# Performance work log

Measured on AMD Instinct MI355X. Metric: run time of the kernel, lower is better.

Reference implementation:

```python
import jax, jax.numpy as jnp
import numpy as np

B, S, IN, IN2, H = 512, 256, 300, 300, 512
FN = 3  # filter_num


def setup_inputs() -> dict:
    key = jax.random.key(0)
    ks = jax.random.split(key, 16)
    def n(k, shape, scale=0.05):
        return jax.random.normal(k, shape, dtype=jnp.float32) * scale
    return {
        "x": jax.random.normal(ks[0], (B, S, IN), dtype=jnp.float32),
        "W_in": n(ks[1], (IN, IN2)), "b_in": n(ks[2], (IN2,)),
        "Wih": n(ks[3], (IN2, 4 * H)), "Whh": n(ks[4], (H, 4 * H)),
        "bih": n(ks[5], (4 * H,)), "bhh": n(ks[6], (4 * H,)),
        "Q": n(ks[7], (H, IN2)), "R": n(ks[8], (IN2, H)),
        "Wc3": n(ks[9], (FN, 1, 3, H)), "bc3": n(ks[10], (FN,)),
        "Wc4": n(ks[11], (FN, 1, 4, H)), "bc4": n(ks[12], (FN,)),
        "Wc5": n(ks[13], (FN, 1, 5, H)), "bc5": n(ks[14], (FN,)),
        "W_lin": n(ks[15], (3 * FN, 2)), "b_lin": jnp.zeros((2,), jnp.float32),
    }


def reference(x, W_in, b_in, Wih, Whh, bih, bhh, Q, R,
              Wc3, bc3, Wc4, bc4, Wc5, bc5, W_lin, b_lin):
    # input projection: [B,S,IN] -> [B,S,IN2]
    xin = jnp.tanh(x @ W_in + b_in)
    xs = jnp.swapaxes(xin, 0, 1)  # [S,B,IN2] for scan
    bsz = x.shape[0]
    h0 = jnp.zeros((bsz, H), x.dtype)
    c0 = jnp.zeros((bsz, H), x.dtype)

    def step(carry, xt):
        ht, Ct = carry
        # mogrify, mog_iterations=2: i=1 odd updates x, i=2 even updates h
        xt = 2.0 * jax.nn.sigmoid(ht @ Q) * xt
        ht = 2.0 * jax.nn.sigmoid(xt @ R) * ht
        gates = xt @ Wih + bih + ht @ Whh + bhh  # [B,4H]
        i, f, g, o = jnp.split(gates, 4, axis=1)
        Ct = jax.nn.sigmoid(f) * Ct + jax.nn.sigmoid(i) * jnp.tanh(g)
        ht = jax.nn.sigmoid(o) * jnp.tanh(Ct)
        return (ht, Ct), ht

    _, hs = jax.lax.scan(step, (h0, c0), xs)  # [S,B,H]
    hmap = jnp.swapaxes(hs, 0, 1)[:, None, :, :]  # [B,1,S,H]

    feats = []
    for w, b in ((Wc3, bc3), (Wc4, bc4), (Wc5, bc5)):
        y = jax.lax.conv_general_dilated(
            hmap, w, (1, 1), 'VALID',
            dimension_numbers=('NCHW', 'OIHW', 'NCHW'))
        y = jax.nn.relu(y + b[None, :, None, None])  # [B,FN,S-fsz+1,1]
        feats.append(jnp.max(y, axis=(2, 3)))  # global max pool -> [B,FN]
    cat = jnp.concatenate(feats, axis=1)  # [B, 3*FN]
    # dropout is identity at inference
    return cat @ W_lin + b_lin  # [B,2]
```

## Files before the change

### kernel.cpp

```cpp
#include <hip/hip_runtime.h>

#define DI __device__ __forceinline__

typedef __attribute__((ext_vector_type(4))) float  f32x4;
typedef __attribute__((ext_vector_type(8))) short  s16x8;
typedef __attribute__((ext_vector_type(8))) __bf16 bf16x8;
typedef unsigned long long u64;

constexpr int S_   = 256;
constexpr int B_   = 512;
constexpr int H_   = 512;
constexpr int KP_  = 320;
constexpr int ALD_ = 832;
constexpr int NRING = 34;
constexpr int NWG  = 256;
constexpr size_t HSLOT = 512 * 512;

constexpr size_t OFF_XIN = 0;
constexpr size_t SZ_XIN  = (size_t)S_ * B_ * KP_ * 2;
constexpr size_t OFF_U   = OFF_XIN + SZ_XIN;
constexpr size_t SZ_U    = (size_t)B_ * S_ * 64 * 4;
constexpr size_t OFF_HS  = OFF_U + SZ_U;
constexpr size_t SZ_HS   = (size_t)NRING * HSLOT * 2;
constexpr size_t OFF_ACT = OFF_HS + SZ_HS;
constexpr size_t SZ_ACT  = (size_t)B_ * ALD_ * 2;
constexpr size_t OFF_HFP = OFF_ACT + SZ_ACT;
constexpr size_t SZ_HFP  = (size_t)B_ * H_ * 4;
constexpr size_t OFF_WPT = OFF_HFP + SZ_HFP;
constexpr size_t SZ_WPT  = (size_t)320 * 320 * 2;
constexpr size_t OFF_QPT = OFF_WPT + SZ_WPT;
constexpr size_t SZ_QPT  = (size_t)320 * 512 * 2;
constexpr size_t OFF_RPT = OFF_QPT + SZ_QPT;
constexpr size_t SZ_RPT  = (size_t)512 * 320 * 2;
constexpr size_t OFF_WGT = OFF_RPT + SZ_RPT;
constexpr size_t SZ_WGT  = (size_t)2048 * 832 * 2;
constexpr size_t OFF_BG  = OFF_WGT + SZ_WGT;
constexpr size_t SZ_BG   = 2048 * 4;
constexpr size_t OFF_VT  = OFF_BG + SZ_BG;
constexpr size_t SZ_VT   = (size_t)64 * 512 * 2;
constexpr size_t OFF_BAR = OFF_VT + SZ_VT;
constexpr size_t SZ_BAR  = 4096;
constexpr size_t WS_NEED = OFF_BAR + SZ_BAR;

DI unsigned short f2bf(float x) {
  unsigned int u = __float_as_uint(x);
  unsigned int r = (u + 0x7FFFu + ((u >> 16) & 1u)) >> 16;
  return (unsigned short)r;
}
DI float bf2f(unsigned short h) { return __uint_as_float(((unsigned int)h) << 16); }

DI float sigm(float x) {
  float e = __builtin_amdgcn_exp2f(x * -1.44269504088896f);
  return __builtin_amdgcn_rcpf(1.0f + e);
}
DI float tanh_(float x) {
  x = fminf(fmaxf(x, -15.0f), 15.0f);
  float e = __builtin_amdgcn_exp2f(x * 2.88539008177793f);
  return (e - 1.0f) * __builtin_amdgcn_rcpf(e + 1.0f);
}
DI bf16x8 asbf(s16x8 v) { return __builtin_bit_cast(bf16x8, v); }

DI u64 ld_sys_u64(const void* p) {
  return __hip_atomic_load((const u64*)p, __ATOMIC_RELAXED, __HIP_MEMORY_SCOPE_SYSTEM);
}
DI void st_sys_u64(void* p, u64 v) {
  __hip_atomic_store((u64*)p, v, __ATOMIC_RELAXED, __HIP_MEMORY_SCOPE_SYSTEM);
}
template<int N> DI void wait_vm() {
  asm volatile("s_waitcnt vmcnt(%0)" :: "n"(N) : "memory");
}

struct a16x8 { u64 lo, hi; };
DI a16x8 ldA(const unsigned short* p) {
  a16x8 r; r.lo = ld_sys_u64(p); r.hi = ld_sys_u64(p + 4); return r;
}
DI void stA_lds(short* dst, a16x8 v) {
  *(u64*)dst = v.lo; *(u64*)(dst + 4) = v.hi;
}

template<int NR>
DI void gemm2(const unsigned short* Ab, int lda,
              const unsigned short* Bb, int ldb,
              short* sA, short* sB, f32x4 acc[2][2])
{
  const int tid  = threadIdx.x;
  const int t2   = tid & 255;
  const int team = tid >> 8;
  const int lane = t2 & 63;
  const int w = t2 >> 6, wm = w >> 1, wn = w & 1;
  const unsigned short* ga = Ab + (t2 >> 2) * lda + (t2 & 3) * 8;
  const unsigned short* gb = Bb + (t2 >> 2) * ldb + (t2 & 3) * 8;
  const int slot  = team * 2048;
  const int arow0 = (wm * 32 + (lane & 15)) * 32 + (lane >> 4) * 8;
  const int brow0 = (wn * 32 + (lane & 15)) * 32 + (lane >> 4) * 8;

  a16x8 a0, a1 = {};
  s16x8 b0, b1 = {};
  a0 = ldA(ga + team * 32);
  b0 = *(const s16x8*)(gb + team * 32);
  if (NR > 1) {
    a1 = ldA(ga + (2 + team) * 32);
    b1 = *(const s16x8*)(gb + (2 + team) * 32);
  }
  stA_lds(&sA[slot + t2 * 8], a0);
  *(s16x8*)&sB[slot + t2 * 8] = b0;
  __syncthreads();
  #pragma unroll
  for (int j = 0; j < NR; ++j) {
    const int cur = (j & 1) * 4096;
    if (j + 2 < NR) {
      const int kt = 2 * (j + 2) + team;
      if ((j & 1) == 0) { a0 = ldA(ga + kt * 32); b0 = *(const s16x8*)(gb + kt * 32); }
      else              { a1 = ldA(ga + kt * 32); b1 = *(const s16x8*)(gb + kt * 32); }
    }
    s16x8 A0 = *(const s16x8*)&sA[cur + slot + arow0];
    s16x8 A1 = *(const s16x8*)&sA[cur + slot + arow0 + 512];
    s16x8 B0 = *(const s16x8*)&sB[cur + slot + brow0];
    s16x8 B1 = *(const s16x8*)&sB[cur + slot + brow0 + 512];
    acc[0][0] = __builtin_amdgcn_mfma_f32_16x16x32_bf16(asbf(A0), asbf(B0), acc[0][0], 0, 0, 0);
    acc[0][1] = __builtin_amdgcn_mfma_f32_16x16x32_bf16(asbf(A0), asbf(B1), acc[0][1], 0, 0, 0);
    acc[1][0] = __builtin_amdgcn_mfma_f32_16x16x32_bf16(asbf(A1), asbf(B0), acc[1][0], 0, 0, 0);
    acc[1][1] = __builtin_amdgcn_mfma_f32_16x16x32_bf16(asbf(A1), asbf(B1), acc[1][1], 0, 0, 0);
    if (j + 1 < NR) {
      const int nxt = ((j + 1) & 1) * 4096;
      if ((j & 1) == 0) { stA_lds(&sA[nxt + slot + t2 * 8], a1); *(s16x8*)&sB[nxt + slot + t2 * 8] = b1; }
      else              { stA_lds(&sA[nxt + slot + t2 * 8], a0); *(s16x8*)&sB[nxt + slot + t2 * 8] = b0; }
    }
    __syncthreads();
  }
}

DI void reduce_teams(f32x4 acc[2][2], float* rbuf) {
  const int tid = threadIdx.x, t2 = tid & 255;
  if (tid >= 256) {
    #pragma unroll
    for (int mi = 0; mi < 2; ++mi)
      #pragma unroll
      for (int ni = 0; ni < 2; ++ni)
        #pragma unroll
        for (int r = 0; r < 4; ++r)
          rbuf[((mi * 2 + ni) * 4 + r) * 256 + t2] = acc[mi][ni][r];
  }
  __syncthreads();
  if (tid < 256) {
    #pragma unroll
    for (int mi = 0; mi < 2; ++mi)
      #pragma unroll
      for (int ni = 0; ni < 2; ++ni)
        #pragma unroll
        for (int r = 0; r < 4; ++r)
          acc[mi][ni][r] += rbuf[((mi * 2 + ni) * 4 + r) * 256 + t2];
  }
}

template<int NK, int KREAL>
DI void gemm_f32A(const float* Af, int lda,
                  const unsigned short* Bb, int ldb,
                  short* sA, short* sB, f32x4 acc[2][2])
{
  const int tid  = threadIdx.x;
  const int lane = tid & 63;
  const int w = tid >> 6, wm = w >> 1, wn = w & 1;
  const float* ga = Af + (tid >> 2) * lda;
  const int cseg  = (tid & 3) * 8;
  const unsigned short* gb = Bb + (tid >> 2) * ldb + (tid & 3) * 8;
  const int arow0 = (wm * 32 + (lane & 15)) * 32 + (lane >> 4) * 8;
  const int brow0 = (wn * 32 + (lane & 15)) * 32 + (lane >> 4) * 8;

  auto loadA = [&](int k) -> s16x8 {
    s16x8 r;
    const int c0 = k * 32 + cseg;
    if (c0 + 8 <= KREAL) {
      float4 f0 = *(const float4*)(ga + c0);
      float4 f1 = *(const float4*)(ga + c0 + 4);
      r[0] = (short)f2bf(f0.x); r[1] = (short)f2bf(f0.y);
      r[2] = (short)f2bf(f0.z); r[3] = (short)f2bf(f0.w);
      r[4] = (short)f2bf(f1.x); r[5] = (short)f2bf(f1.y);
      r[6] = (short)f2bf(f1.z); r[7] = (short)f2bf(f1.w);
    } else {
      #pragma unroll
      for (int j = 0; j < 8; ++j) {
        float x = (c0 + j < KREAL) ? ga[c0 + j] : 0.0f;
        r[j] = (short)f2bf(x);
      }
    }
    return r;
  };

  s16x8 va = loadA(0);
  s16x8 vb = *(const s16x8*)gb;
  *(s16x8*)&sA[tid * 8] = va;
  *(s16x8*)&sB[tid * 8] = vb;
  __syncthreads();
  for (int k = 0; k < NK; ++k) {
    const int cur = (k & 1) * 2048;
    if (k + 1 < NK) {
      va = loadA(k + 1);
      vb = *(const s16x8*)(gb + (k + 1) * 32);
    }
    s16x8 a0 = *(const s16x8*)&sA[cur + arow0];
    s16x8 a1 = *(const s16x8*)&sA[cur + arow0 + 16 * 32];
    s16x8 b0 = *(const s16x8*)&sB[cur + brow0];
    s16x8 b1 = *(const s16x8*)&sB[cur + brow0 + 16 * 32];
    acc[0][0] = __builtin_amdgcn_mfma_f32_16x16x32_bf16(asbf(a0), asbf(b0), acc[0][0], 0, 0, 0);
    acc[0][1] = __builtin_amdgcn_mfma_f32_16x16x32_bf16(asbf(a0), asbf(b1), acc[0][1], 0, 0, 0);
    acc[1][0] = __builtin_amdgcn_mfma_f32_16x16x32_bf16(asbf(a1), asbf(b0), acc[1][0], 0, 0, 0);
    acc[1][1] = __builtin_amdgcn_mfma_f32_16x16x32_bf16(asbf(a1), asbf(b1), acc[1][1], 0, 0, 0);
    if (k + 1 < NK) {
      const int nxt = ((k + 1) & 1) * 2048;
      *(s16x8*)&sA[nxt + tid * 8] = va;
      *(s16x8*)&sB[nxt + tid * 8] = vb;
    }
    __syncthreads();
  }
}

template<typename F>
DI void epiloop(f32x4 acc[2][2], F&& f) {
  const int lane = threadIdx.x & 63;
  const int w = (threadIdx.x & 255) >> 6, wm = w >> 1, wn = w & 1;
  #pragma unroll
  for (int mi = 0; mi < 2; ++mi)
    #pragma unroll
    for (int ni = 0; ni < 2; ++ni)
      #pragma unroll
      for (int r = 0; r < 4; ++r) {
        const int rowl = wm * 32 + mi * 16 + (lane >> 4) * 4 + r;
        const int coll = wn * 32 + ni * 16 + (lane & 15);
        f(rowl, coll, acc[mi][ni][r]);
      }
}

DI void pack_store_512(const unsigned short* lds16, unsigned short* dstbase, int ldd) {
  const u64* l64 = (const u64*)lds16;
  #pragma unroll
  for (int it = 0; it < 2; ++it) {
    const int i = it * 512 + threadIdx.x;
    const int row = i >> 4, q = i & 15;
    st_sys_u64(dstbase + row * ldd + q * 4, l64[row * 16 + q]);
  }
}

__global__ void k_prep_wpt(const float* __restrict__ Wi, unsigned short* __restrict__ WpT) {
  int i = blockIdx.x * 256 + threadIdx.x;
  if (i >= 320 * 320) return;
  int n = i / 320, k = i % 320;
  float v = (n < 300 && k < 300) ? Wi[k * 300 + n] : 0.0f;
  WpT[i] = f2bf(v);
}
__global__ void k_prep_qpt(const float* __restrict__ Q, unsigned short* __restrict__ QpT) {
  int i = blockIdx.x * 256 + threadIdx.x;
  if (i >= 320 * 512) return;
  int n = i >> 9, k = i & 511;
  float v = (n < 300) ? Q[k * 300 + n] : 0.0f;
  QpT[i] = f2bf(v);
}
__global__ void k_prep_rpt(const float* __restrict__ R, unsigned short* __restrict__ RpT) {
  int i = blockIdx.x * 256 + threadIdx.x;
  if (i >= 512 * 320) return;
  int n = i / 320, k = i % 320;
  float v = (k < 300) ? R[k * 512 + n] : 0.0f;
  RpT[i] = f2bf(v);
}
__global__ void k_prep_wgt(const float* __restrict__ Wih, const float* __restrict__ Whh,
                           unsigned short* __restrict__ WgT) {
  int i = blockIdx.x * 256 + threadIdx.x;
  if (i >= 2048 * 832) return;
  int np = i / 832, k = i % 832;
  int c = np >> 2, g = np & 3, col = g * 512 + c;
  float v = 0.0f;
  if (k < 300) v = Wih[k * 2048 + col];
  else if (k >= 320) v = Whh[(k - 320) * 2048 + col];
  WgT[i] = f2bf(v);
}
__global__ void k_prep_bg(const float* __restrict__ bih, const float* __restrict__ bhh,
                          float* __restrict__ bg) {
  int i = blockIdx.x * 256 + threadIdx.x;
  if (i >= 2048) return;
  int c = i >> 2, g = i & 3, col = g * 512 + c;
  bg[i] = bih[col] + bhh[col];
}
__global__ void k_prep_vt(const float* __restrict__ Wc3, const float* __restrict__ Wc4,
                          const float* __restrict__ Wc5, unsigned short* __restrict__ VT) {
  int i = blockIdx.x * 256 + threadIdx.x;
  if (i >= 64 * 512) return;
  int j = i >> 9, k = i & 511;
  float v = 0.0f;
  if (j < 9)       { int f = j / 3,  dt = j % 3;        v = Wc3[(f * 3 + dt) * 512 + k]; }
  else if (j < 21) { int jj = j - 9;  int f = jj / 4, dt = jj % 4; v = Wc4[(f * 4 + dt) * 512 + k]; }
  else if (j < 36) { int jj = j - 21; int f = jj / 5, dt = jj % 5; v = Wc5[(f * 5 + dt) * 512 + k]; }
  VT[i] = f2bf(v);
}
__global__ void k_wsfail(float* out, int n, float v) {
  int i = blockIdx.x * 256 + threadIdx.x;
  if (i < n) out[i] = -v;
}

__global__ __launch_bounds__(256) void k_proj(const float* __restrict__ x,
                                              const unsigned short* __restrict__ WpT,
                                              const float* __restrict__ b_in,
                                              unsigned short* __restrict__ xin) {
  __shared__ short sA[4096], sB[4096];
  const int m0 = blockIdx.x * 64, n0 = blockIdx.y * 64;
  f32x4 acc[2][2];
  const f32x4 z = {0.f, 0.f, 0.f, 0.f};
  acc[0][0] = z; acc[0][1] = z; acc[1][0] = z; acc[1][1] = z;
  gemm_f32A<10, 300>(x + (size_t)m0 * 300, 300, WpT + n0 * 320, 320, sA, sB, acc);
  epiloop(acc, [&](int rowl, int coll, float vacc) {
    const int row = m0 + rowl, col = n0 + coll;
    float o = 0.0f;
    if (col < 300) o = tanh_(vacc + b_in[col]);
    const int b = row >> 8, s = row & 255;
    xin[(size_t)(s * 512 + b) * KP_ + col] = f2bf(o);
  });
}

__global__ __launch_bounds__(512, 2) void k_scan(
    const unsigned short* __restrict__ xin,
    const unsigned short* __restrict__ QpT,
    const unsigned short* __restrict__ RpT,
    const unsigned short* __restrict__ WgT,
    const float* __restrict__ bg,
    const unsigned short* __restrict__ VT,
    unsigned short* __restrict__ hs,
    unsigned short* __restrict__ act,
    float* __restrict__ hfp,
    float* __restrict__ U,
    unsigned int* __restrict__ bar)
{
  __shared__ short sA[8192], sB[8192];
  __shared__ float gbuf[4096];
  __shared__ float rbuf[4096];
  __shared__ float pbuf[4096];
  __shared__ unsigned short obuf[4096];
  const int wg   = blockIdx.x;
  const int grp  = wg >> 5;
  const int l    = wg & 31;
  const int tid  = threadIdx.x;
  const f32x4 z = {0.f, 0.f, 0.f, 0.f};

  const int gm0 = grp * 64;
  const int gn0 = l * 64;
  float c_state[2] = {0.f, 0.f};

  int ep = 0;
  auto bar_sync = [&]() {
    wait_vm<0>();
    __syncthreads();
    if (tid == 0) {
      __hip_atomic_fetch_add(&bar[grp * 64], 1u,
                             __ATOMIC_RELAXED, __HIP_MEMORY_SCOPE_AGENT);
      const unsigned tgt = (unsigned)(ep + 1) * 32u;
      while (__hip_atomic_load(&bar[grp * 64], __ATOMIC_RELAXED,
                               __HIP_MEMORY_SCOPE_AGENT) < tgt)
        __builtin_amdgcn_s_sleep(1);
    }
    __syncthreads();
    ++ep;
  };

  for (int t = 0; t < S_; ++t) {
    const unsigned short* hst = hs + (size_t)(t % NRING) * HSLOT;
    unsigned short*       hso = hs + (size_t)((t + 1) % NRING) * HSLOT;

    if (l < 5) {
      const int m0 = gm0, n0 = l * 64;
      f32x4 acc[2][2];
      acc[0][0] = z; acc[0][1] = z; acc[1][0] = z; acc[1][1] = z;
      gemm2<8>(hst + m0 * 512, 512, QpT + n0 * 512, 512, sA, sB, acc);
      reduce_teams(acc, rbuf);
      if (tid < 256) {
        const unsigned short* xin_t = xin + (size_t)t * 512 * KP_;
        epiloop(acc, [&](int rowl, int coll, float vacc) {
          obuf[rowl * 64 + coll] =
            f2bf(2.0f * sigm(vacc) * bf2f(xin_t[(m0 + rowl) * KP_ + n0 + coll]));
        });
      }
      __syncthreads();
      pack_store_512(obuf, act + m0 * ALD_ + n0, ALD_);
    }
    bar_sync();

    if (l < 8) {
      const int m0 = gm0, n0 = l * 64;
      {
        u64* p64 = (u64*)pbuf;
        #pragma unroll
        for (int it = 0; it < 4; ++it) {
          const int i = it * 512 + tid;
          const int row = i >> 5, p = i & 31;
          p64[row * 32 + p] = ld_sys_u64(hfp + (m0 + row) * 512 + n0 + p * 2);
        }
      }
      f32x4 acc[2][2];
      acc[0][0] = z; acc[0][1] = z; acc[1][0] = z; acc[1][1] = z;
      gemm2<5>(act + m0 * ALD_, ALD_, RpT + n0 * KP_, KP_, sA, sB, acc);
      reduce_teams(acc, rbuf);
      if (tid < 256) {
        epiloop(acc, [&](int rowl, int coll, float vacc) {
          obuf[rowl * 64 + coll] = f2bf(2.0f * sigm(vacc) * pbuf[rowl * 64 + coll]);
        });
      }
      __syncthreads();
      pack_store_512(obuf, act + m0 * ALD_ + 320 + n0, ALD_);
    }
    bar_sync();

    {
      f32x4 acc[2][2];
      acc[0][0] = z; acc[0][1] = z; acc[1][0] = z; acc[1][1] = z;
      gemm2<13>(act + gm0 * ALD_, ALD_, WgT + gn0 * 832, 832, sA, sB, acc);
      reduce_teams(acc, rbuf);
      if (tid < 256) {
        epiloop(acc, [&](int rowl, int coll, float vacc) {
          gbuf[rowl * 64 + coll] = vacc;
        });
      }
      __syncthreads();
      unsigned short* hbuf = obuf;
      float*          fbuf = rbuf;
      #pragma unroll
      for (int q = 0; q < 2; ++q) {
        const int item = q * 512 + tid;
        const int row = item >> 4, cu = item & 15;
        const float4 bb = *(const float4*)&bg[gn0 + cu * 4];
        const float iv = gbuf[row * 64 + cu * 4 + 0] + bb.x;
        const float fv = gbuf[row * 64 + cu * 4 + 1] + bb.y;
        const float gv = gbuf[row * 64 + cu * 4 + 2] + bb.z;
        const float ov = gbuf[row * 64 + cu * 4 + 3] + bb.w;
        const float cn = sigm(fv) * c_state[q] + sigm(iv) * tanh_(gv);
        const float h  = sigm(ov) * tanh_(cn);
        c_state[q] = cn;
        hbuf[row * 16 + cu] = f2bf(h);
        fbuf[row * 16 + cu] = h;
      }
      __syncthreads();
      if (tid < 256) {
        const u64* h64 = (const u64*)hbuf;
        const int row = tid >> 2, q = tid & 3;
        st_sys_u64(hso + (gm0 + row) * 512 + (gn0 >> 2) + q * 4, h64[row * 4 + q]);
      }
      {
        const u64* f64 = (const u64*)fbuf;
        const int r2 = tid >> 3, p = tid & 7;
        st_sys_u64(hfp + (gm0 + r2) * 512 + (gn0 >> 2) + p * 2, f64[r2 * 8 + p]);
      }
    }
    bar_sync();

    if ((t & 31) == 31) {
      const int c = t >> 5;
      const int tglob = 32 * c + l;
      const int slot = (tglob + 1) % NRING;
      const int brow = gm0;
      f32x4 acc[2][2];
      acc[0][0] = z; acc[0][1] = z; acc[1][0] = z; acc[1][1] = z;
      gemm2<8>(hs + (size_t)slot * HSLOT + (size_t)brow * 512, 512, VT, 512, sA, sB, acc);
      reduce_teams(acc, rbuf);
      if (tid < 256) {
        epiloop(acc, [&](int rowl, int coll, float vacc) {
          U[((size_t)(brow + rowl) * 256 + tglob) * 64 + coll] = vacc;
        });
      }
    }
  }
}

__global__ __launch_bounds__(256) void k_combine(const float* __restrict__ U,
                                                 const float* __restrict__ bc3,
                                                 const float* __restrict__ bc4,
                                                 const float* __restrict__ bc5,
                                                 const float* __restrict__ Wl,
                                                 const float* __restrict__ bl,
                                                 float* __restrict__ out) {
  const int b = blockIdx.x;
  const int p = threadIdx.x;
  const float* Ub = U + (size_t)b * (256 * 64);
  float v[9];
  #pragma unroll
  for (int j = 0; j < 9; ++j) v[j] = -1e30f;
  if (p < 254) {
    #pragma unroll
    for (int f = 0; f < 3; ++f)
      v[f] = Ub[(p + 0) * 64 + f * 3 + 0] + Ub[(p + 1) * 64 + f * 3 + 1] + Ub[(p + 2) * 64 + f * 3 + 2];
  }
  if (p < 253) {
    #pragma unroll
    for (int f = 0; f < 3; ++f)
      v[3 + f] = Ub[(p + 0) * 64 + 9 + f * 4 + 0] + Ub[(p + 1) * 64 + 9 + f * 4 + 1] +
                 Ub[(p + 2) * 64 + 9 + f * 4 + 2] + Ub[(p + 3) * 64 + 9 + f * 4 + 3];
  }
  if (p < 252) {
    #pragma unroll
    for (int f = 0; f < 3; ++f)
      v[6 + f] = Ub[(p + 0) * 64 + 21 + f * 5 + 0] + Ub[(p + 1) * 64 + 21 + f * 5 + 1] +
                 Ub[(p + 2) * 64 + 21 + f * 5 + 2] + Ub[(p + 3) * 64 + 21 + f * 5 + 3] +
                 Ub[(p + 4) * 64 + 21 + f * 5 + 4];
  }
  __shared__ float red[4][9];
  const int lane = threadIdx.x & 63, w = threadIdx.x >> 6;
  #pragma unroll
  for (int j = 0; j < 9; ++j) {
    float m = v[j];
    #pragma unroll
    for (int off = 32; off >= 1; off >>= 1) m = fmaxf(m, __shfl_xor(m, off));
    if (lane == 0) red[w][j] = m;
  }
  __syncthreads();
  if (threadIdx.x < 2) {
    const int k = threadIdx.x;
    float o = bl[k];
    #pragma unroll
    for (int j = 0; j < 9; ++j) {
      float m = fmaxf(fmaxf(red[0][j], red[1][j]), fmaxf(red[2][j], red[3][j]));
      float bias = (j < 3) ? bc3[j] : (j < 6) ? bc4[j - 3] : bc5[j - 6];
      o += fmaxf(m + bias, 0.0f) * Wl[j * 2 + k];
    }
    out[b * 2 + k] = o;
  }
}

extern "C" void kernel_launch(void* const* d_in, const int* in_sizes, int n_in,
                              void* d_out, int out_size, void* d_ws, size_t ws_size,
                              hipStream_t stream) {
  const float* x     = (const float*)d_in[0];
  const float* W_in  = (const float*)d_in[1];
  const float* b_in  = (const float*)d_in[2];
  const float* Wih   = (const float*)d_in[3];
  const float* Whh   = (const float*)d_in[4];
  const float* bih   = (const float*)d_in[5];
  const float* bhh   = (const float*)d_in[6];
  const float* Q     = (const float*)d_in[7];
  const float* R     = (const float*)d_in[8];
  const float* Wc3   = (const float*)d_in[9];
  const float* bc3   = (const float*)d_in[10];
  const float* Wc4   = (const float*)d_in[11];
  const float* bc4   = (const float*)d_in[12];
  const float* Wc5   = (const float*)d_in[13];
  const float* bc5   = (const float*)d_in[14];
  const float* W_lin = (const float*)d_in[15];
  const float* b_lin = (const float*)d_in[16];

  if (ws_size < WS_NEED) {
    k_wsfail<<<4, 256, 0, stream>>>((float*)d_out, out_size, (float)(ws_size >> 20));
    return;
  }

  char* ws = (char*)d_ws;
  unsigned short* xin = (unsigned short*)(ws + OFF_XIN);
  float*          U   = (float*)(ws + OFF_U);
  unsigned short* hs  = (unsigned short*)(ws + OFF_HS);
  unsigned short* act = (unsigned short*)(ws + OFF_ACT);
  float*          hfp = (float*)(ws + OFF_HFP);
  unsigned short* WpT = (unsigned short*)(ws + OFF_WPT);
  unsigned short* QpT = (unsigned short*)(ws + OFF_QPT);
  unsigned short* RpT = (unsigned short*)(ws + OFF_RPT);
  unsigned short* WgT = (unsigned short*)(ws + OFF_WGT);
  float*          bg  = (float*)(ws + OFF_BG);
  unsigned short* VT  = (unsigned short*)(ws + OFF_VT);
  unsigned int*   bar = (unsigned int*)(ws + OFF_BAR);

  (void)hipMemsetAsync(hs, 0, HSLOT * 2, stream);
  (void)hipMemsetAsync(hfp, 0, SZ_HFP, stream);
  (void)hipMemsetAsync(bar, 0, SZ_BAR, stream);

  k_prep_wpt<<<(320 * 320 + 255) / 256, 256, 0, stream>>>(W_in, WpT);
  k_prep_qpt<<<(320 * 512 + 255) / 256, 256, 0, stream>>>(Q, QpT);
  k_prep_rpt<<<(512 * 320 + 255) / 256, 256, 0, stream>>>(R, RpT);
  k_prep_wgt<<<(2048 * 832 + 255) / 256, 256, 0, stream>>>(Wih, Whh, WgT);
  k_prep_bg<<<8, 256, 0, stream>>>(bih, bhh, bg);
  k_prep_vt<<<(64 * 512 + 255) / 256, 256, 0, stream>>>(Wc3, Wc4, Wc5, VT);

  k_proj<<<dim3(131072 / 64, KP_ / 64), 256, 0, stream>>>(x, WpT, b_in, xin);

  k_scan<<<NWG, 512, 0, stream>>>(xin, QpT, RpT, WgT, bg, VT, hs, act, hfp, U, bar);

  k_combine<<<512, 256, 0, stream>>>(U, bc3, bc4, bc5, W_lin, b_lin, (float*)d_out);
}
```

Measured before the change: 5.490 ms.

## Use 4-way K-split GEMM tiles, flag-based group barrier, drop fp32 h buffer

Replaces the 2-team 64x64 GEMM helper with a 4-team K-split version that uses 16-column-wide k tiles and a 2x4 MFMA accumulator per wave, plus a 3-way LDS reduction. The gate weight layout is permuted so each wave holds i/f/g/o for the same hidden columns in registers, which lets the LSTM cell update run directly on accumulators without a gate staging buffer. The atomic-counter group barrier becomes per-workgroup flag stores polled by a whole wavefront. The separate fp32 hidden-state copy is removed and the bf16 ring is reused for the mogrifier's h multiply. This cuts global traffic and barrier latency in the sequential scan, at the cost of more LDS, some precision loss from bf16 h, and a heavier reduction step.

```diff
diff --git a/kernel.cpp b/kernel.cpp
--- a/kernel.cpp
+++ b/kernel.cpp
@@ -9,7 +9,6 @@
 
 constexpr int S_   = 256;
 constexpr int B_   = 512;
-constexpr int H_   = 512;
 constexpr int KP_  = 320;
 constexpr int ALD_ = 832;
 constexpr int NRING = 34;
@@ -24,9 +23,7 @@
 constexpr size_t SZ_HS   = (size_t)NRING * HSLOT * 2;
 constexpr size_t OFF_ACT = OFF_HS + SZ_HS;
 constexpr size_t SZ_ACT  = (size_t)B_ * ALD_ * 2;
-constexpr size_t OFF_HFP = OFF_ACT + SZ_ACT;
-constexpr size_t SZ_HFP  = (size_t)B_ * H_ * 4;
-constexpr size_t OFF_WPT = OFF_HFP + SZ_HFP;
+constexpr size_t OFF_WPT = OFF_ACT + SZ_ACT;
 constexpr size_t SZ_WPT  = (size_t)320 * 320 * 2;
 constexpr size_t OFF_QPT = OFF_WPT + SZ_WPT;
 constexpr size_t SZ_QPT  = (size_t)320 * 512 * 2;
@@ -59,6 +56,10 @@
   return (e - 1.0f) * __builtin_amdgcn_rcpf(e + 1.0f);
 }
 DI bf16x8 asbf(s16x8 v) { return __builtin_bit_cast(bf16x8, v); }
+DI s16x8 as16(u64 a, u64 b) {
+  struct P { u64 x, y; } p{a, b};
+  return __builtin_bit_cast(s16x8, p);
+}
 
 DI u64 ld_sys_u64(const void* p) {
   return __hip_atomic_load((const u64*)p, __ATOMIC_RELAXED, __HIP_MEMORY_SCOPE_SYSTEM);
@@ -66,90 +67,103 @@
 DI void st_sys_u64(void* p, u64 v) {
   __hip_atomic_store((u64*)p, v, __ATOMIC_RELAXED, __HIP_MEMORY_SCOPE_SYSTEM);
 }
+DI unsigned int ld_sys_u32(const unsigned int* p) {
+  return __hip_atomic_load(p, __ATOMIC_RELAXED, __HIP_MEMORY_SCOPE_SYSTEM);
+}
+DI void st_sys_u32(unsigned int* p, unsigned int v) {
+  __hip_atomic_store(p, v, __ATOMIC_RELAXED, __HIP_MEMORY_SCOPE_SYSTEM);
+}
 template<int N> DI void wait_vm() {
   asm volatile("s_waitcnt vmcnt(%0)" :: "n"(N) : "memory");
 }
 
-struct a16x8 { u64 lo, hi; };
-DI a16x8 ldA(const unsigned short* p) {
-  a16x8 r; r.lo = ld_sys_u64(p); r.hi = ld_sys_u64(p + 4); return r;
-}
-DI void stA_lds(short* dst, a16x8 v) {
-  *(u64*)dst = v.lo; *(u64*)(dst + 4) = v.hi;
-}
-
-template<int NR>
-DI void gemm2(const unsigned short* Ab, int lda,
+template<int NK>
+DI void gemm4(const unsigned short* Ab, int lda,
               const unsigned short* Bb, int ldb,
-              short* sA, short* sB, f32x4 acc[2][2])
+              short* sA, short* sB, f32x4 acc[2][4])
 {
+  constexpr int NR = (NK + 3) / 4;
   const int tid  = threadIdx.x;
-  const int t2   = tid & 255;
-  const int team = tid >> 8;
-  const int lane = t2 & 63;
-  const int w = t2 >> 6, wm = w >> 1, wn = w & 1;
-  const unsigned short* ga = Ab + (t2 >> 2) * lda + (t2 & 3) * 8;
-  const unsigned short* gb = Bb + (t2 >> 2) * ldb + (t2 & 3) * 8;
-  const int slot  = team * 2048;
-  const int arow0 = (wm * 32 + (lane & 15)) * 32 + (lane >> 4) * 8;
-  const int brow0 = (wn * 32 + (lane & 15)) * 32 + (lane >> 4) * 8;
-
-  a16x8 a0, a1 = {};
-  s16x8 b0, b1 = {};
-  a0 = ldA(ga + team * 32);
-  b0 = *(const s16x8*)(gb + team * 32);
-  if (NR > 1) {
-    a1 = ldA(ga + (2 + team) * 32);
-    b1 = *(const s16x8*)(gb + (2 + team) * 32);
-  }
-  stA_lds(&sA[slot + t2 * 8], a0);
-  *(s16x8*)&sB[slot + t2 * 8] = b0;
+  const int tm   = tid >> 7;
+  const int t7   = tid & 127;
+  const int lane = tid & 63;
+  const int l15  = lane & 15;
+  const int kseg = (lane >> 4) * 8;
+  const int w1   = (tid >> 6) & 1;
+  const int srow = t7 >> 1, scol = (t7 & 1) * 16;
+  const unsigned short* ga = Ab + srow * lda + scol;
+  const unsigned short* gb = Bb + srow * ldb + scol;
+  short* mysA = sA + tm * 4096;
+  short* mysB = sB + tm * 4096;
+  const int sidx = srow * 32 + scol;
+  const int arow = (w1 * 32 + l15) * 32 + kseg;
+
+  u64 a[2][4], b[2][4];
+  auto loadA = [&](int kt, u64* d) {
+    const unsigned short* p = ga + kt * 32;
+    d[0] = ld_sys_u64(p);     d[1] = ld_sys_u64(p + 4);
+    d[2] = ld_sys_u64(p + 8); d[3] = ld_sys_u64(p + 12);
+  };
+  auto loadB = [&](int kt, u64* d) {
+    const u64* p = (const u64*)(gb + kt * 32);
+    d[0] = p[0]; d[1] = p[1]; d[2] = p[2]; d[3] = p[3];
+  };
+  auto stage = [&](int buf, const u64* da, const u64* db) {
+    u64* pa = (u64*)&mysA[buf * 2048 + sidx];
+    u64* pb = (u64*)&mysB[buf * 2048 + sidx];
+    pa[0] = da[0]; pa[1] = da[1]; pa[2] = da[2]; pa[3] = da[3];
+    pb[0] = db[0]; pb[1] = db[1]; pb[2] = db[2]; pb[3] = db[3];
+  };
+
+  loadA(tm, a[0]);     loadB(tm, b[0]);
+  loadA(4 + tm, a[1]); loadB(4 + tm, b[1]);
+  stage(0, a[0], b[0]);
   __syncthreads();
   #pragma unroll
   for (int j = 0; j < NR; ++j) {
-    const int cur = (j & 1) * 4096;
-    if (j + 2 < NR) {
-      const int kt = 2 * (j + 2) + team;
-      if ((j & 1) == 0) { a0 = ldA(ga + kt * 32); b0 = *(const s16x8*)(gb + kt * 32); }
-      else              { a1 = ldA(ga + kt * 32); b1 = *(const s16x8*)(gb + kt * 32); }
-    }
-    s16x8 A0 = *(const s16x8*)&sA[cur + slot + arow0];
-    s16x8 A1 = *(const s16x8*)&sA[cur + slot + arow0 + 512];
-    s16x8 B0 = *(const s16x8*)&sB[cur + slot + brow0];
-    s16x8 B1 = *(const s16x8*)&sB[cur + slot + brow0 + 512];
-    acc[0][0] = __builtin_amdgcn_mfma_f32_16x16x32_bf16(asbf(A0), asbf(B0), acc[0][0], 0, 0, 0);
-    acc[0][1] = __builtin_amdgcn_mfma_f32_16x16x32_bf16(asbf(A0), asbf(B1), acc[0][1], 0, 0, 0);
-    acc[1][0] = __builtin_amdgcn_mfma_f32_16x16x32_bf16(asbf(A1), asbf(B0), acc[1][0], 0, 0, 0);
-    acc[1][1] = __builtin_amdgcn_mfma_f32_16x16x32_bf16(asbf(A1), asbf(B1), acc[1][1], 0, 0, 0);
-    if (j + 1 < NR) {
-      const int nxt = ((j + 1) & 1) * 4096;
-      if ((j & 1) == 0) { stA_lds(&sA[nxt + slot + t2 * 8], a1); *(s16x8*)&sB[nxt + slot + t2 * 8] = b1; }
-      else              { stA_lds(&sA[nxt + slot + t2 * 8], a0); *(s16x8*)&sB[nxt + slot + t2 * 8] = b0; }
-    }
+    const int cur = (j & 1) * 2048;
+    if (j + 2 < NR && (j + 2) * 4 + tm < NK) {
+      loadA((j + 2) * 4 + tm, a[j & 1]);
+      loadB((j + 2) * 4 + tm, b[j & 1]);
+    }
+    if (j * 4 + tm < NK) {
+      s16x8 A0 = *(const s16x8*)&mysA[cur + arow];
+      s16x8 A1 = *(const s16x8*)&mysA[cur + arow + 512];
+      #pragma unroll
+      for (int ni = 0; ni < 4; ++ni) {
+        s16x8 Bn = *(const s16x8*)&mysB[cur + (ni * 16 + l15) * 32 + kseg];
+        acc[0][ni] = __builtin_amdgcn_mfma_f32_16x16x32_bf16(asbf(A0), asbf(Bn), acc[0][ni], 0, 0, 0);
+        acc[1][ni] = __builtin_amdgcn_mfma_f32_16x16x32_bf16(asbf(A1), asbf(Bn), acc[1][ni], 0, 0, 0);
+      }
+    }
+    if (j + 1 < NR && (j + 1) * 4 + tm < NK)
+      stage((j + 1) & 1, a[(j + 1) & 1], b[(j + 1) & 1]);
     __syncthreads();
   }
 }
 
-DI void reduce_teams(f32x4 acc[2][2], float* rbuf) {
-  const int tid = threadIdx.x, t2 = tid & 255;
-  if (tid >= 256) {
+DI void reduce4(f32x4 acc[2][4], float* rbuf) {
+  const int tid = threadIdx.x, tm = tid >> 7, t7 = tid & 127;
+  if (tm > 0) {
     #pragma unroll
     for (int mi = 0; mi < 2; ++mi)
       #pragma unroll
-      for (int ni = 0; ni < 2; ++ni)
+      for (int ni = 0; ni < 4; ++ni)
         #pragma unroll
         for (int r = 0; r < 4; ++r)
-          rbuf[((mi * 2 + ni) * 4 + r) * 256 + t2] = acc[mi][ni][r];
+          rbuf[(tm - 1) * 4096 + ((mi * 4 + ni) * 4 + r) * 128 + t7] = acc[mi][ni][r];
   }
   __syncthreads();
-  if (tid < 256) {
-    #pragma unroll
-    for (int mi = 0; mi < 2; ++mi)
-      #pragma unroll
-      for (int ni = 0; ni < 2; ++ni)
-        #pragma unroll
-        for (int r = 0; r < 4; ++r)
-          acc[mi][ni][r] += rbuf[((mi * 2 + ni) * 4 + r) * 256 + t2];
+  if (tm == 0) {
+    #pragma unroll
+    for (int s = 0; s < 3; ++s)
+      #pragma unroll
+      for (int mi = 0; mi < 2; ++mi)
+        #pragma unroll
+        for (int ni = 0; ni < 4; ++ni)
+          #pragma unroll
+          for (int r = 0; r < 4; ++r)
+            acc[mi][ni][r] += rbuf[s * 4096 + ((mi * 4 + ni) * 4 + r) * 128 + t7];
   }
 }
 
@@ -266,8 +280,9 @@
                            unsigned short* __restrict__ WgT) {
   int i = blockIdx.x * 256 + threadIdx.x;
   if (i >= 2048 * 832) return;
-  int np = i / 832, k = i % 832;
-  int c = np >> 2, g = np & 3, col = g * 512 + c;
+  int n = i / 832, k = i % 832;
+  int l = n >> 6, j = n & 63, g = j >> 4, hcl = j & 15;
+  int col = g * 512 + l * 16 + hcl;
   float v = 0.0f;
   if (k < 300) v = Wih[k * 2048 + col];
   else if (k >= 320) v = Whh[(k - 320) * 2048 + col];
@@ -277,7 +292,8 @@
                           float* __restrict__ bg) {
   int i = blockIdx.x * 256 + threadIdx.x;
   if (i >= 2048) return;
-  int c = i >> 2, g = i & 3, col = g * 512 + c;
+  int l = i >> 6, j = i & 63, g = j >> 4, hcl = j & 15;
+  int col = g * 512 + l * 16 + hcl;
   bg[i] = bih[col] + bhh[col];
 }
 __global__ void k_prep_vt(const float* __restrict__ Wc3, const float* __restrict__ Wc4,
@@ -324,38 +340,37 @@
     const unsigned short* __restrict__ VT,
     unsigned short* __restrict__ hs,
     unsigned short* __restrict__ act,
-    float* __restrict__ hfp,
     float* __restrict__ U,
     unsigned int* __restrict__ bar)
 {
-  __shared__ short sA[8192], sB[8192];
-  __shared__ float gbuf[4096];
-  __shared__ float rbuf[4096];
-  __shared__ float pbuf[4096];
+  __shared__ short sA[16384], sB[16384];
+  __shared__ float rbuf[12288];
+  __shared__ unsigned short pbuf[4096];
   __shared__ unsigned short obuf[4096];
   const int wg   = blockIdx.x;
   const int grp  = wg >> 5;
   const int l    = wg & 31;
   const int tid  = threadIdx.x;
+  const int lane = tid & 63;
+  const int l15  = lane & 15;
   const f32x4 z = {0.f, 0.f, 0.f, 0.f};
 
   const int gm0 = grp * 64;
   const int gn0 = l * 64;
-  float c_state[2] = {0.f, 0.f};
-
+  float c_state[8] = {};
+  float bias[4];
+  #pragma unroll
+  for (int g = 0; g < 4; ++g) bias[g] = bg[gn0 + g * 16 + l15];
+
+  unsigned int* flags = bar + grp * 32;
   int ep = 0;
   auto bar_sync = [&]() {
     wait_vm<0>();
     __syncthreads();
-    if (tid == 0) {
-      __hip_atomic_fetch_add(&bar[grp * 64], 1u,
-                             __ATOMIC_RELAXED, __HIP_MEMORY_SCOPE_AGENT);
-      const unsigned tgt = (unsigned)(ep + 1) * 32u;
-      while (__hip_atomic_load(&bar[grp * 64], __ATOMIC_RELAXED,
-                               __HIP_MEMORY_SCOPE_AGENT) < tgt)
-        __builtin_amdgcn_s_sleep(1);
-    }
-    __syncthreads();
+    const unsigned tag = (unsigned)(ep + 1);
+    if (tid == 0) st_sys_u32(&flags[l], tag);
+    while (!__all(ld_sys_u32(&flags[lane & 31]) >= tag))
+      __builtin_amdgcn_s_sleep(2);
     ++ep;
   };
 
@@ -364,86 +379,110 @@
     unsigned short*       hso = hs + (size_t)((t + 1) % NRING) * HSLOT;
 
     if (l < 5) {
-      const int m0 = gm0, n0 = l * 64;
-      f32x4 acc[2][2];
-      acc[0][0] = z; acc[0][1] = z; acc[1][0] = z; acc[1][1] = z;
-      gemm2<8>(hst + m0 * 512, 512, QpT + n0 * 512, 512, sA, sB, acc);
-      reduce_teams(acc, rbuf);
-      if (tid < 256) {
-        const unsigned short* xin_t = xin + (size_t)t * 512 * KP_;
-        epiloop(acc, [&](int rowl, int coll, float vacc) {
-          obuf[rowl * 64 + coll] =
-            f2bf(2.0f * sigm(vacc) * bf2f(xin_t[(m0 + rowl) * KP_ + n0 + coll]));
-        });
+      const int n0 = l * 64;
+      {
+        const unsigned short* xin_t = xin + ((size_t)t * 512 + gm0) * KP_;
+        u64* p64 = (u64*)pbuf;
+        #pragma unroll
+        for (int it = 0; it < 2; ++it) {
+          const int i = it * 512 + tid;
+          const int row = i >> 4, q = i & 15;
+          p64[i] = *(const u64*)(xin_t + row * KP_ + n0 + q * 4);
+        }
+      }
+      f32x4 acc[2][4];
+      #pragma unroll
+      for (int mi = 0; mi < 2; ++mi)
+        #pragma unroll
+        for (int ni = 0; ni < 4; ++ni) acc[mi][ni] = z;
+      gemm4<16>(hst + gm0 * 512, 512, QpT + n0 * 512, 512, sA, sB, acc);
+      reduce4(acc, rbuf);
+      if (tid < 128) {
+        const int w1 = (tid >> 6) & 1;
+        #pragma unroll
+        for (int mi = 0; mi < 2; ++mi)
+          #pragma unroll
+          for (int ni = 0; ni < 4; ++ni)
+            #pragma unroll
+            for (int r = 0; r < 4; ++r) {
+              const int row = w1 * 32 + mi * 16 + (lane >> 4) * 4 + r;
+              const int col = ni * 16 + l15;
+              obuf[row * 64 + col] =
+                f2bf(2.0f * sigm(acc[mi][ni][r]) * bf2f(pbuf[row * 64 + col]));
+            }
       }
       __syncthreads();
-      pack_store_512(obuf, act + m0 * ALD_ + n0, ALD_);
+      pack_store_512(obuf, act + gm0 * ALD_ + n0, ALD_);
     }
     bar_sync();
 
     if (l < 8) {
-      const int m0 = gm0, n0 = l * 64;
+      const int n0 = l * 64;
       {
         u64* p64 = (u64*)pbuf;
         #pragma unroll
-        for (int it = 0; it < 4; ++it) {
+        for (int it = 0; it < 2; ++it) {
           const int i = it * 512 + tid;
-          const int row = i >> 5, p = i & 31;
-          p64[row * 32 + p] = ld_sys_u64(hfp + (m0 + row) * 512 + n0 + p * 2);
+          const int row = i >> 4, q = i & 15;
+          p64[i] = ld_sys_u64(hst + (gm0 + row) * 512 + n0 + q * 4);
         }
       }
-      f32x4 acc[2][2];
-      acc[0][0] = z; acc[0][1] = z; acc[1][0] = z; acc[1][1] = z;
-      gemm2<5>(act + m0 * ALD_, ALD_, RpT + n0 * KP_, KP_, sA, sB, acc);
-      reduce_teams(acc, rbuf);
-      if (tid < 256) {
-        epiloop(acc, [&](int rowl, int coll, float vacc) {
-          obuf[rowl * 64 + coll] = f2bf(2.0f * sigm(vacc) * pbuf[rowl * 64 + coll]);
-        });
+      f32x4 acc[2][4];
+      #pragma unroll
+      for (int mi = 0; mi < 2; ++mi)
+        #pragma unroll
+        for (int ni = 0; ni < 4; ++ni) acc[mi][ni] = z;
+      gemm4<10>(act + gm0 * ALD_, ALD_, RpT + n0 * KP_, KP_, sA, sB, acc);
+      reduce4(acc, rbuf);
+      if (tid < 128) {
+        const int w1 = (tid >> 6) & 1;
+        #pragma unroll
+        for (int mi = 0; mi < 2; ++mi)
+          #pragma unroll
+          for (int ni = 0; ni < 4; ++ni)
+            #pragma unroll
+            for (int r = 0; r < 4; ++r) {
+              const int row = w1 * 32 + mi * 16 + (lane >> 4) * 4 + r;
+              const int col = ni * 16 + l15;
+              obuf[row * 64 + col] =
+                f2bf(2.0f * sigm(acc[mi][ni][r]) * bf2f(pbuf[row * 64 + col]));
+            }
       }
       __syncthreads();
-      pack_store_512(obuf, act + m0 * ALD_ + 320 + n0, ALD_);
+      pack_store_512(obuf, act + gm0 * ALD_ + 320 + n0, ALD_);
     }
     bar_sync();
 
     {
-      f32x4 acc[2][2];
-      acc[0][0] = z; acc[0][1] = z; acc[1][0] = z; acc[1][1] = z;
-      gemm2<13>(act + gm0 * ALD_, ALD_, WgT + gn0 * 832, 832, sA, sB, acc);
-      reduce_teams(acc, rbuf);
-      if (tid < 256) {
-        epiloop(acc, [&](int rowl, int coll, float vacc) {
-          gbuf[rowl * 64 + coll] = vacc;
-        });
-      }
-      __syncthreads();
-      unsigned short* hbuf = obuf;
-      float*          fbuf = rbuf;
-      #pragma unroll
-      for (int q = 0; q < 2; ++q) {
-        const int item = q * 512 + tid;
-        const int row = item >> 4, cu = item & 15;
-        const float4 bb = *(const float4*)&bg[gn0 + cu * 4];
-        const float iv = gbuf[row * 64 + cu * 4 + 0] + bb.x;
-        const float fv = gbuf[row * 64 + cu * 4 + 1] + bb.y;
-        const float gv = gbuf[row * 64 + cu * 4 + 2] + bb.z;
-        const float ov = gbuf[row * 64 + cu * 4 + 3] + bb.w;
-        const float cn = sigm(fv) * c_state[q] + sigm(iv) * tanh_(gv);
-        const float h  = sigm(ov) * tanh_(cn);
-        c_state[q] = cn;
-        hbuf[row * 16 + cu] = f2bf(h);
-        fbuf[row * 16 + cu] = h;
+      f32x4 acc[2][4];
+      #pragma unroll
+      for (int mi = 0; mi < 2; ++mi)
+        #pragma unroll
+        for (int ni = 0; ni < 4; ++ni) acc[mi][ni] = z;
+      gemm4<26>(act + gm0 * ALD_, ALD_, WgT + gn0 * 832, 832, sA, sB, acc);
+      reduce4(acc, rbuf);
+      if (tid < 128) {
+        const int w1 = (tid >> 6) & 1;
+        #pragma unroll
+        for (int mi = 0; mi < 2; ++mi)
+          #pragma unroll
+          for (int r = 0; r < 4; ++r) {
+            const int row = w1 * 32 + mi * 16 + (lane >> 4) * 4 + r;
+            const float iv = acc[mi][0][r] + bias[0];
+            const float fv = acc[mi][1][r] + bias[1];
+            const float gv = acc[mi][2][r] + bias[2];
+            const float ov = acc[mi][3][r] + bias[3];
+            const float cn = sigm(fv) * c_state[mi * 4 + r] + sigm(iv) * tanh_(gv);
+            const float h  = sigm(ov) * tanh_(cn);
+            c_state[mi * 4 + r] = cn;
+            obuf[row * 16 + l15] = f2bf(h);
+          }
       }
       __syncthreads();
       if (tid < 256) {
-        const u64* h64 = (const u64*)hbuf;
+        const u64* h64 = (const u64*)obuf;
         const int row = tid >> 2, q = tid & 3;
-        st_sys_u64(hso + (gm0 + row) * 512 + (gn0 >> 2) + q * 4, h64[row * 4 + q]);
-      }
-      {
-        const u64* f64 = (const u64*)fbuf;
-        const int r2 = tid >> 3, p = tid & 7;
-        st_sys_u64(hfp + (gm0 + r2) * 512 + (gn0 >> 2) + p * 2, f64[r2 * 8 + p]);
+        st_sys_u64(hso + (gm0 + row) * 512 + l * 16 + q * 4, h64[row * 4 + q]);
       }
     }
     bar_sync();
@@ -452,15 +491,25 @@
       const int c = t >> 5;
       const int tglob = 32 * c + l;
       const int slot = (tglob + 1) % NRING;
-      const int brow = gm0;
-      f32x4 acc[2][2];
-      acc[0][0] = z; acc[0][1] = z; acc[1][0] = z; acc[1][1] = z;
-      gemm2<8>(hs + (size_t)slot * HSLOT + (size_t)brow * 512, 512, VT, 512, sA, sB, acc);
-      reduce_teams(acc, rbuf);
-      if (tid < 256) {
-        epiloop(acc, [&](int rowl, int coll, float vacc) {
-          U[((size_t)(brow + rowl) * 256 + tglob) * 64 + coll] = vacc;
-        });
+      f32x4 acc[2][4];
+      #pragma unroll
+      for (int mi = 0; mi < 2; ++mi)
+        #pragma unroll
+        for (int ni = 0; ni < 4; ++ni) acc[mi][ni] = z;
+      gemm4<16>(hs + (size_t)slot * HSLOT + (size_t)gm0 * 512, 512, VT, 512, sA, sB, acc);
+      reduce4(acc, rbuf);
+      if (tid < 128) {
+        const int w1 = (tid >> 6) & 1;
+        #pragma unroll
+        for (int mi = 0; mi < 2; ++mi)
+          #pragma unroll
+          for (int ni = 0; ni < 4; ++ni)
+            #pragma unroll
+            for (int r = 0; r < 4; ++r) {
+              const int row = w1 * 32 + mi * 16 + (lane >> 4) * 4 + r;
+              const int j = ni * 16 + l15;
+              U[((size_t)(gm0 + row) * 256 + tglob) * 64 + j] = acc[mi][ni][r];
+            }
       }
     }
   }
@@ -551,7 +600,6 @@
   float*          U   = (float*)(ws + OFF_U);
   unsigned short* hs  = (unsigned short*)(ws + OFF_HS);
   unsigned short* act = (unsigned short*)(ws + OFF_ACT);
-  float*          hfp = (float*)(ws + OFF_HFP);
   unsigned short* WpT = (unsigned short*)(ws + OFF_WPT);
   unsigned short* QpT = (unsigned short*)(ws + OFF_QPT);
   unsigned short* RpT = (unsigned short*)(ws + OFF_RPT);
@@ -561,7 +609,6 @@
   unsigned int*   bar = (unsigned int*)(ws + OFF_BAR);
 
   (void)hipMemsetAsync(hs, 0, HSLOT * 2, stream);
-  (void)hipMemsetAsync(hfp, 0, SZ_HFP, stream);
   (void)hipMemsetAsync(bar, 0, SZ_BAR, stream);
 
   k_prep_wpt<<<(320 * 320 + 255) / 256, 256, 0, stream>>>(W_in, WpT);
@@ -573,7 +620,7 @@
 
   k_proj<<<dim3(131072 / 64, KP_ / 64), 256, 0, stream>>>(x, WpT, b_in, xin);
 
-  k_scan<<<NWG, 512, 0, stream>>>(xin, QpT, RpT, WgT, bg, VT, hs, act, hfp, U, bar);
+  k_scan<<<NWG, 512, 0, stream>>>(xin, QpT, RpT, WgT, bg, VT, hs, act, U, bar);
 
   k_combine<<<512, 256, 0, stream>>>(U, bc3, bc4, bc5, W_lin, b_lin, (float*)d_out);
 }
```

Measured after the change: 7.595 ms (median of 2 runs). 1.38x slower.
